# Kernel tuning notes

Hardware: AMD Instinct MI355X
Metric: run time of the kernel (lower is better)

The kernel has to match this reference:

```python
import jax, jax.numpy as jnp
import numpy as np

N = 100000   # num_entities
R = 474      # num_relations (already doubled for inverses)
D = 256      # in_dim == out_dim
E = 1000000  # num edges (first half 'in' mode, second half 'out' mode)
BN_EPS = 1e-5


def setup_inputs() -> dict:
    key = jax.random.key(0)
    ks = jax.random.split(key, 12)
    s = 1.0 / np.sqrt(D)
    return {
        "x": jax.random.normal(ks[0], (N, D), jnp.float32),
        "r": jax.random.normal(ks[1], (R, D), jnp.float32),
        "w_in": jax.random.normal(ks[2], (D, D), jnp.float32) * s,
        "w_out": jax.random.normal(ks[3], (D, D), jnp.float32) * s,
        "w_loop": jax.random.normal(ks[4], (D, D), jnp.float32) * s,
        "w_rel": jax.random.normal(ks[5], (D, D), jnp.float32) * s,
        "loop_rel": jax.random.normal(ks[6], (1, D), jnp.float32),
        "bias": jnp.zeros((D,), jnp.float32),
        "bn_gamma": jnp.ones((D,), jnp.float32),
        "bn_beta": jnp.zeros((D,), jnp.float32),
        "edge_index": jax.random.randint(ks[7], (2, E), 0, N, jnp.int32),
        "edge_type": jax.random.randint(ks[8], (E,), 0, R, jnp.int32),
    }


def reference(x, r, w_in, w_out, w_loop, w_rel, loop_rel, bias,
              bn_gamma, bn_beta, edge_index, edge_type):
    row, col = edge_index[0], edge_index[1]
    # symmetric edge norm 1/(sqrt(D_i) sqrt(D_j)); degrees over all edges
    deg = jax.ops.segment_sum(jnp.ones((E,), x.dtype), row, num_segments=N)
    deg_inv = jnp.where(deg > 0, deg ** -0.5, 0.0)
    norm = deg_inv[row] * deg_inv[col]  # [E]

    r_full = jnp.concatenate([r, loop_rel], axis=0)  # [R+1, D]

    def mode_agg(rw, cl, et, nrm, W):
        # gather -> composition (sub) -> per-mode matmul -> edge-norm -> scatter-add
        composed = x[cl] - r_full[et]                  # [e, D]
        msg = (composed @ W) * nrm[:, None]            # [e, D]
        return jax.ops.segment_sum(msg, rw, num_segments=N)

    half = edge_type.shape[0] // 2
    agg_in = mode_agg(row[:half], col[:half], edge_type[:half], norm[:half], w_in)
    agg_out = mode_agg(row[half:], col[half:], edge_type[half:], norm[half:], w_out)
    # self-loop: every node, relation = loop_rel (no edge norm)
    agg_loop = (x - loop_rel) @ w_loop                 # [N, D]

    h = agg_in + agg_out + agg_loop + bias
    # BatchNorm1d over node dim (batch statistics)
    mean = jnp.mean(h, axis=0)
    var = jnp.var(h, axis=0)
    h = bn_gamma * (h - mean) * jax.lax.rsqrt(var + BN_EPS) + bn_beta
    h = jnp.tanh(h)

    r_out = r @ w_rel  # rel_transformation == 'linear'
    return h, r_out
```

## Files before the change

kernel.cpp:

```cpp
#include <hip/hip_runtime.h>
#include <hip/hip_bf16.h>
#include <stdint.h>

#define D_DIM 256
#define KBIG 768

typedef __attribute__((ext_vector_type(8))) short bf16x8_t;
typedef __attribute__((ext_vector_type(4))) float f32x4_t;
typedef __attribute__((ext_vector_type(2))) float f32x2_t;

__device__ __forceinline__ float bf2f(uint16_t u) {
    union { uint32_t i; float f; } v; v.i = ((uint32_t)u) << 16; return v.f;
}
__device__ __forceinline__ uint16_t f2bf(float f) {
    union { float f; uint32_t i; } v; v.f = f;
    uint32_t x = v.i;
    uint32_t r = (x + 0x7FFFu + ((x >> 16) & 1u)) >> 16;
    return (uint16_t)r;
}
__device__ __forceinline__ uint32_t pack2(float a, float b) {
    return (uint32_t)f2bf(a) | ((uint32_t)f2bf(b) << 16);
}
__device__ __forceinline__ float loadv(const void* base, int f, size_t idx) {
    return f ? ((const float*)base)[idx] : bf2f(((const uint16_t*)base)[idx]);
}
__device__ __forceinline__ float fast_tanh(float x) {
    float t = __builtin_amdgcn_exp2f(x * 2.8853900817779268f);
    return 1.f - 2.f * __builtin_amdgcn_rcpf(t + 1.f);
}
__device__ __forceinline__ f32x2_t up2(uint32_t w) {
    union { uint32_t u[2]; f32x2_t f; } c;
    c.u[0] = w << 16;
    c.u[1] = w & 0xFFFF0000u;
    return c.f;
}
__device__ __forceinline__ void pkfma(f32x2_t& acc, f32x2_t a, f32x2_t b) {
    asm("v_pk_fma_f32 %0, %1, %2, %0" : "+v"(acc) : "v"(a), "v"(b));
}

__device__ __forceinline__ void gll16(const uint16_t* g, uint16_t* l) {
    __builtin_amdgcn_global_load_lds(
        (const __attribute__((address_space(1))) uint32_t*)(const void*)g,
        (__attribute__((address_space(3))) uint32_t*)(void*)l, 16, 0, 0);
}

__global__ void k_detect(const uint32_t* __restrict__ xw, int* __restrict__ flag) {
    int lane = threadIdx.x;
    int c = 0;
#pragma unroll
    for (int j = 0; j < 8; j++) {
        uint32_t w = xw[(size_t)(lane * 8 + j) * 6151];
        uint32_t e = (w >> 7) & 0xFF;
        c += (e >= 100 && e <= 140) ? 1 : 0;
    }
#pragma unroll
    for (int off = 32; off; off >>= 1) c += __shfl_down(c, off);
    if (lane == 0) flag[0] = (c < 128) ? 1 : 0;
}

__global__ __launch_bounds__(256) void k_cast(const void* __restrict__ src,
                                              uint16_t* __restrict__ dst,
                                              int nvec, const int* __restrict__ flagp,
                                              int skip_bf) {
    int f = *flagp;
    int i = blockIdx.x * 256 + threadIdx.x;
    if (i >= nvec) return;
    size_t base = (size_t)i * 8;
    if (f) {
        const float* s = (const float*)src + base;
        float4 a = *(const float4*)s;
        float4 b = *(const float4*)(s + 4);
        uint4 o;
        o.x = (uint32_t)f2bf(a.x) | ((uint32_t)f2bf(a.y) << 16);
        o.y = (uint32_t)f2bf(a.z) | ((uint32_t)f2bf(a.w) << 16);
        o.z = (uint32_t)f2bf(b.x) | ((uint32_t)f2bf(b.y) << 16);
        o.w = (uint32_t)f2bf(b.z) | ((uint32_t)f2bf(b.w) << 16);
        *(uint4*)(dst + base) = o;
    } else {
        if (skip_bf) return;
        *(uint4*)(dst + base) = *(const uint4*)((const uint16_t*)src + base);
    }
}

__global__ void k_transpose(const void* __restrict__ w0, const void* __restrict__ w1,
                            const void* __restrict__ w2, const void* __restrict__ w3,
                            const int* __restrict__ flagp,
                            uint16_t* __restrict__ bt_big, uint16_t* __restrict__ bt_rel) {
    __shared__ uint16_t tile[32][33];
    int f = *flagp;
    int mat = blockIdx.z;
    const void* src = mat == 0 ? w0 : mat == 1 ? w1 : mat == 2 ? w2 : w3;
    int k0 = blockIdx.y * 32, n0 = blockIdx.x * 32;
    int tx = threadIdx.x, ty = threadIdx.y;
    tile[ty][tx] = f2bf(loadv(src, f, (size_t)(k0 + ty) * D_DIM + n0 + tx));
    __syncthreads();
    int n = n0 + ty, k = k0 + tx;
    if (mat < 3) bt_big[(size_t)n * KBIG + mat * D_DIM + k] = tile[tx][ty];
    else         bt_rel[(size_t)n * D_DIM + k] = tile[tx][ty];
}

__global__ void k_cvec(const void* __restrict__ loop_rel, const void* __restrict__ w_loop,
                       const void* __restrict__ bias, const int* __restrict__ flagp,
                       float* __restrict__ cvec) {
    int f = *flagp;
    int c = blockIdx.x;
    int lane = threadIdx.x;
    float s = 0.f;
#pragma unroll
    for (int kk = 0; kk < 4; kk++) {
        int k = kk * 64 + lane;
        s += loadv(loop_rel, f, k) * loadv(w_loop, f, (size_t)k * D_DIM + c);
    }
#pragma unroll
    for (int off = 32; off; off >>= 1) s += __shfl_down(s, off);
    if (lane == 0) cvec[c] = loadv(bias, f, c) - s;
}

__global__ void k_hist(const int* __restrict__ rows, int E, int half,
                       int* __restrict__ deg) {
    int i = blockIdx.x * blockDim.x + threadIdx.x;
    if (i < E) atomicAdd(&deg[rows[i]], (i < half) ? 0x10001 : 1);
}

__global__ void k_scan_a(const int* __restrict__ deg, int N, int* __restrict__ row_start,
                         int* __restrict__ blk_sum, float* __restrict__ dinv) {
    __shared__ int s[1024];
    int t = threadIdx.x;
    int i = blockIdx.x * 1024 + t;
    int v = (i < N) ? (deg[i] & 0xFFFF) : 0;
    if (i < N) dinv[i] = v > 0 ? rsqrtf((float)v) : 0.f;
    s[t] = v;
    __syncthreads();
    for (int off = 1; off < 1024; off <<= 1) {
        int add = (t >= off) ? s[t - off] : 0;
        __syncthreads();
        s[t] += add;
        __syncthreads();
    }
    if (i < N) row_start[i] = s[t] - v;
    if (t == 1023) blk_sum[blockIdx.x] = s[1023];
}

__global__ void k_scan_b(int* __restrict__ blk_sum, int nb) {
    __shared__ int s[128];
    int t = threadIdx.x;
    int v = (t < nb) ? blk_sum[t] : 0;
    s[t] = v;
    __syncthreads();
    for (int off = 1; off < 128; off <<= 1) {
        int add = (t >= off) ? s[t - off] : 0;
        __syncthreads();
        s[t] += add;
        __syncthreads();
    }
    if (t < nb) blk_sum[t] = s[t] - v;
}

__global__ void k_scan_c(int* __restrict__ row_start, const int* __restrict__ blk_sum,
                         const int* __restrict__ degp,
                         int N, int E, int* __restrict__ cur_in, int* __restrict__ cur_out) {
    int i = blockIdx.x * 1024 + threadIdx.x;
    if (i < N) {
        int v = row_start[i] + blk_sum[blockIdx.x];
        row_start[i] = v;
        cur_in[i] = v;
        cur_out[i] = v + (int)(((unsigned)degp[i]) >> 16);
    }
    if (i == 0) row_start[N] = E;
}

__global__ void k_fill(const int* __restrict__ ei, const int* __restrict__ et, int E, int half,
                       int* __restrict__ cur_in, int* __restrict__ cur_out,
                       const float* __restrict__ dinv, uint2* __restrict__ csr) {
    int e = blockIdx.x * blockDim.x + threadIdx.x;
    if (e >= E) return;
    int r_ = ei[e];
    int c_ = ei[E + e];
    int t_ = et[e];
    float w = dinv[r_] * dinv[c_];
    uint32_t m = ((uint32_t)c_ << 9) | (uint32_t)t_;
    int pos = (e < half) ? atomicAdd(&cur_in[r_], 1) : atomicAdd(&cur_out[r_], 1);
    csr[pos] = make_uint2(m, __float_as_uint(w));
}

__global__ __launch_bounds__(256) void k_agg(
    const uint2* __restrict__ csr, const int* __restrict__ row_start,
    const int* __restrict__ degp,
    const void* __restrict__ x_raw, const uint16_t* __restrict__ x_bf,
    const uint16_t* __restrict__ r_bf, const int* __restrict__ flagp,
    uint16_t* __restrict__ s_in, uint16_t* __restrict__ s_out, int N) {
    const char* xb = (const char*)((*flagp) ? x_bf : (const uint16_t*)x_raw);
    const char* rb = (const char*)r_bf;
    int node = blockIdx.x * 4 + (threadIdx.x >> 6);
    int lane = threadIdx.x & 63;
    if (node >= N) return;
    int half = lane >> 5;
    int cob = (lane & 31) * 16;
    int s = row_start[node], e = row_start[node + 1];
    int mid = s + (int)(((unsigned)degp[node]) >> 16);

    f32x2_t ax[4], ar[4];
    float a[8];

#pragma unroll
    for (int k = 0; k < 4; k++) { ax[k] = (f32x2_t){0.f, 0.f}; ar[k] = (f32x2_t){0.f, 0.f}; }
    for (int j = s + half; j < mid; j += 2) {
        uint2 rec = csr[j];
        uint32_t m = rec.x;
        float w = __uint_as_float(rec.y);
        uint4 xv = *(const uint4*)(xb + (m & 0xFFFFFE00u) + cob);
        uint4 rv = *(const uint4*)(rb + ((m & 511u) << 9) + cob);
        f32x2_t w2 = {w, w};
        pkfma(ax[0], up2(xv.x), w2); pkfma(ar[0], up2(rv.x), w2);
        pkfma(ax[1], up2(xv.y), w2); pkfma(ar[1], up2(rv.y), w2);
        pkfma(ax[2], up2(xv.z), w2); pkfma(ar[2], up2(rv.z), w2);
        pkfma(ax[3], up2(xv.w), w2); pkfma(ar[3], up2(rv.w), w2);
    }
#pragma unroll
    for (int k = 0; k < 4; k++) { a[2 * k] = ax[k][0] - ar[k][0]; a[2 * k + 1] = ax[k][1] - ar[k][1]; }
#pragma unroll
    for (int k = 0; k < 8; k++) a[k] += __shfl_xor(a[k], 32);
    if (half == 0) {
        uint4 o;
        o.x = pack2(a[0], a[1]); o.y = pack2(a[2], a[3]);
        o.z = pack2(a[4], a[5]); o.w = pack2(a[6], a[7]);
        *(uint4*)(s_in + (size_t)node * D_DIM + (cob >> 1)) = o;
    }

#pragma unroll
    for (int k = 0; k < 4; k++) { ax[k] = (f32x2_t){0.f, 0.f}; ar[k] = (f32x2_t){0.f, 0.f}; }
    for (int j = mid + half; j < e; j += 2) {
        uint2 rec = csr[j];
        uint32_t m = rec.x;
        float w = __uint_as_float(rec.y);
        uint4 xv = *(const uint4*)(xb + (m & 0xFFFFFE00u) + cob);
        uint4 rv = *(const uint4*)(rb + ((m & 511u) << 9) + cob);
        f32x2_t w2 = {w, w};
        pkfma(ax[0], up2(xv.x), w2); pkfma(ar[0], up2(rv.x), w2);
        pkfma(ax[1], up2(xv.y), w2); pkfma(ar[1], up2(rv.y), w2);
        pkfma(ax[2], up2(xv.z), w2); pkfma(ar[2], up2(rv.z), w2);
        pkfma(ax[3], up2(xv.w), w2); pkfma(ar[3], up2(rv.w), w2);
    }
#pragma unroll
    for (int k = 0; k < 4; k++) { a[2 * k] = ax[k][0] - ar[k][0]; a[2 * k + 1] = ax[k][1] - ar[k][1]; }
#pragma unroll
    for (int k = 0; k < 8; k++) a[k] += __shfl_xor(a[k], 32);
    if (half == 1) {
        uint4 o;
        o.x = pack2(a[0], a[1]); o.y = pack2(a[2], a[3]);
        o.z = pack2(a[4], a[5]); o.w = pack2(a[6], a[7]);
        *(uint4*)(s_out + (size_t)node * D_DIM + (cob >> 1)) = o;
    }
}

__global__ __launch_bounds__(512) void k_gemm(
    const uint16_t* a0, const uint16_t* a1,
    const uint16_t* a2, const uint16_t* a2alt, const int* __restrict__ flagp,
    int M, const uint16_t* __restrict__ bt, int bstride, int ktot,
    const float* __restrict__ addvec, uint16_t* out,
    float* __restrict__ bn_sum, float* __restrict__ bn_sq,
    void* __restrict__ dout2, long long d_off) {
    __shared__ uint16_t As[2][128 * 32];
    __shared__ uint16_t Bs[2][256 * 32];
    int fl = *flagp;
    const uint16_t* a2s = fl ? a2 : a2alt;
    int t = threadIdx.x;
    int mbase = blockIdx.x * 128;
    int wave = t >> 6, lane = t & 63;
    int wm = (wave >> 2) * 64, wn = (wave & 3) * 64;
    int quad = lane >> 4, l15 = lane & 15;

    int roff = lane >> 2, cidx = lane & 3;
    int arowL = wave * 16 + roff;
    int achk = cidx ^ ((arowL >> 1) & 3);
    int agrow = mbase + arowL; if (agrow > M - 1) agrow = M - 1;
    size_t aoff = (size_t)agrow * D_DIM + achk * 8;
    int awoff = (wave * 16) * 32;

    int browL0 = wave * 32 + roff;
    int browL1 = browL0 + 16;
    int bchk0 = cidx ^ ((browL0 >> 1) & 3);
    int bchk1 = cidx ^ ((browL1 >> 1) & 3);
    size_t boff0 = (size_t)browL0 * bstride + bchk0 * 8;
    size_t boff1 = (size_t)browL1 * bstride + bchk1 * 8;
    int bwoff0 = (wave * 32) * 32;
    int bwoff1 = (wave * 32 + 16) * 32;

    int afo[4], bfo[4];
#pragma unroll
    for (int im = 0; im < 4; im++) {
        int row = wm + im * 16 + l15;
        afo[im] = row * 32 + (quad ^ ((row >> 1) & 3)) * 8;
    }
#pragma unroll
    for (int in = 0; in < 4; in++) {
        int row = wn + in * 16 + l15;
        bfo[in] = row * 32 + (quad ^ ((row >> 1) & 3)) * 8;
    }

    f32x4_t acc[4][4];
#pragma unroll
    for (int i = 0; i < 4; i++)
#pragma unroll
        for (int j = 0; j < 4; j++) acc[i][j] = (f32x4_t){0.f, 0.f, 0.f, 0.f};

    auto stage = [&](int buf, int kt) {
        const uint16_t* asec = (kt < 256) ? a0 : (kt < 512 ? a1 : a2s);
        gll16(asec + aoff + (kt & 255), &As[buf][awoff]);
        gll16(bt + boff0 + kt, &Bs[buf][bwoff0]);
        gll16(bt + boff1 + kt, &Bs[buf][bwoff1]);
    };

    stage(0, 0);
    int cur = 0;
    for (int kt = 0; kt < ktot; kt += 32) {
        if (kt + 32 < ktot) {
            stage(cur ^ 1, kt + 32);
            asm volatile("s_waitcnt vmcnt(3)" ::: "memory");
        } else {
            asm volatile("s_waitcnt vmcnt(0)" ::: "memory");
        }
        __builtin_amdgcn_sched_barrier(0);
        __builtin_amdgcn_s_barrier();
        bf16x8_t af[4], bfr[4];
#pragma unroll
        for (int im = 0; im < 4; im++) af[im] = *(const bf16x8_t*)(&As[cur][afo[im]]);
#pragma unroll
        for (int in = 0; in < 4; in++) bfr[in] = *(const bf16x8_t*)(&Bs[cur][bfo[in]]);
#pragma unroll
        for (int im = 0; im < 4; im++)
#pragma unroll
            for (int in = 0; in < 4; in++)
                acc[im][in] = __builtin_amdgcn_mfma_f32_16x16x32_bf16(af[im], bfr[in], acc[im][in], 0, 0, 0);
        asm volatile("s_waitcnt lgkmcnt(0)" ::: "memory");
        __builtin_amdgcn_sched_barrier(0);
        __builtin_amdgcn_s_barrier();
        cur ^= 1;
    }

    float s4[4] = {0.f, 0.f, 0.f, 0.f};
    float q4[4] = {0.f, 0.f, 0.f, 0.f};
#pragma unroll
    for (int im = 0; im < 4; im++) {
#pragma unroll
        for (int in = 0; in < 4; in++) {
            int gn = wn + in * 16 + l15;
            float av_ = addvec ? addvec[gn] : 0.f;
#pragma unroll
            for (int i2 = 0; i2 < 4; i2++) {
                int gm = mbase + wm + im * 16 + quad * 4 + i2;
                if (gm < M) {
                    float val = acc[im][in][i2] + av_;
                    if (dout2) {
                        size_t idx = (size_t)d_off + (size_t)gm * D_DIM + gn;
                        if (fl) ((float*)dout2)[idx] = val;
                        else    ((uint16_t*)dout2)[idx] = f2bf(val);
                    } else {
                        out[(size_t)gm * D_DIM + gn] = f2bf(val);
                    }
                    if (bn_sum) { s4[in] += val; q4[in] += val * val; }
                }
            }
        }
    }
    if (bn_sum) {
        float* sred = (float*)&As[0][0];
        __syncthreads();
        if (t < 256) { sred[t] = 0.f; sred[t + 256] = 0.f; }
        __syncthreads();
#pragma unroll
        for (int in = 0; in < 4; in++) {
            float sv = s4[in], qv = q4[in];
            sv += __shfl_xor(sv, 16); sv += __shfl_xor(sv, 32);
            qv += __shfl_xor(qv, 16); qv += __shfl_xor(qv, 32);
            if (quad == 0) {
                int gn = wn + in * 16 + l15;
                atomicAdd(&sred[gn], sv);
                atomicAdd(&sred[gn + 256], qv);
            }
        }
        __syncthreads();
        if (t < 256) {
            atomicAdd(&bn_sum[t], sred[t]);
            atomicAdd(&bn_sq[t], sred[t + 256]);
        }
    }
}

__global__ __launch_bounds__(256) void k_final(const uint16_t* __restrict__ h_pre,
                                               const float* __restrict__ bn_sum,
                                               const float* __restrict__ bn_sq,
                                               const void* __restrict__ gamma,
                                               const void* __restrict__ beta,
                                               const int* __restrict__ flagp,
                                               int N, void* __restrict__ dout, int total) {
    __shared__ float ssc[256], ssh[256];
    int f = *flagp;
    {
        int c = threadIdx.x;
        float inv_n = 1.f / (float)N;
        float mean = bn_sum[c] * inv_n;
        float var = bn_sq[c] * inv_n - mean * mean;
        float sc = loadv(gamma, f, c) * rsqrtf(var + 1e-5f);
        ssc[c] = sc;
        ssh[c] = loadv(beta, f, c) - mean * sc;
    }
    __syncthreads();
    int t = blockIdx.x * 256 + threadIdx.x;
    int base = t * 8;
    if (base >= total) return;
    int c0 = base & (D_DIM - 1);
    uint4 v = *(const uint4*)(h_pre + base);
    uint16_t e[8];
    e[0] = (uint16_t)(v.x & 0xFFFF); e[1] = (uint16_t)(v.x >> 16);
    e[2] = (uint16_t)(v.y & 0xFFFF); e[3] = (uint16_t)(v.y >> 16);
    e[4] = (uint16_t)(v.z & 0xFFFF); e[5] = (uint16_t)(v.z >> 16);
    e[6] = (uint16_t)(v.w & 0xFFFF); e[7] = (uint16_t)(v.w >> 16);
    float r[8];
#pragma unroll
    for (int i = 0; i < 8; i++)
        r[i] = fast_tanh(bf2f(e[i]) * ssc[c0 + i] + ssh[c0 + i]);
    if (f) {
        float* fo = (float*)dout + base;
        float4 o0 = {r[0], r[1], r[2], r[3]};
        float4 o1 = {r[4], r[5], r[6], r[7]};
        *(float4*)fo = o0;
        *(float4*)(fo + 4) = o1;
    } else {
        uint4 o;
        o.x = (uint32_t)f2bf(r[0]) | ((uint32_t)f2bf(r[1]) << 16);
        o.y = (uint32_t)f2bf(r[2]) | ((uint32_t)f2bf(r[3]) << 16);
        o.z = (uint32_t)f2bf(r[4]) | ((uint32_t)f2bf(r[5]) << 16);
        o.w = (uint32_t)f2bf(r[6]) | ((uint32_t)f2bf(r[7]) << 16);
        *(uint4*)((uint16_t*)dout + base) = o;
    }
}

extern "C" void kernel_launch(void* const* d_in, const int* in_sizes, int n_in,
                              void* d_out, int out_size, void* d_ws, size_t ws_size,
                              hipStream_t stream) {
    const void* x        = d_in[0];
    const void* r        = d_in[1];
    const void* w_in     = d_in[2];
    const void* w_out    = d_in[3];
    const void* w_loop   = d_in[4];
    const void* w_rel    = d_in[5];
    const void* loop_rel = d_in[6];
    const void* bias     = d_in[7];
    const void* bn_gamma = d_in[8];
    const void* bn_beta  = d_in[9];
    const int* edge_index = (const int*)d_in[10];
    const int* edge_type  = (const int*)d_in[11];

    const int N = in_sizes[0] / D_DIM;
    const int R = in_sizes[1] / D_DIM;
    const int E = in_sizes[11];
    const int half = E / 2;

    char* p = (char*)d_ws;
    auto alloc = [&](size_t bytes) -> void* {
        void* q = (void*)p;
        p += (bytes + 255) & ~(size_t)255;
        return q;
    };
    uint16_t* s_out   = (uint16_t*)alloc((size_t)N * D_DIM * 2);
    uint2*    csr     = (uint2*)alloc((size_t)E * 8);
    uint16_t* bt_big  = (uint16_t*)alloc((size_t)D_DIM * KBIG * 2);
    uint16_t* bt_rel  = (uint16_t*)alloc((size_t)D_DIM * D_DIM * 2);
    uint16_t* r_bf    = (uint16_t*)alloc((size_t)R * D_DIM * 2 + 65536);
    int*      deg     = (int*)alloc((size_t)N * 4);
    int*      rstart  = (int*)alloc((size_t)(N + 1) * 4);
    int*      cursor  = (int*)alloc((size_t)N * 4);
    int*      cursor_out = (int*)alloc((size_t)N * 4);
    float*    dinv    = (float*)alloc((size_t)N * 4);
    int*      blksum  = (int*)alloc(128 * 4);
    float*    cvec    = (float*)alloc(D_DIM * 4);
    float*    bn_sum  = (float*)alloc(D_DIM * 4);
    float*    bn_sq   = (float*)alloc(D_DIM * 4);
    int*      dflag   = (int*)alloc(256);
    (void)bn_sq;

    uint16_t* s_in = (uint16_t*)d_out;
    uint16_t* x_bf = (uint16_t*)d_out + (size_t)N * D_DIM;
    uint16_t* h_pre = s_out;

    hipMemsetAsync(deg, 0, (size_t)N * 4, stream);
    hipMemsetAsync(bn_sum, 0, 2 * D_DIM * 4, stream);

    k_detect<<<1, 64, 0, stream>>>((const uint32_t*)x, dflag);
    int xvec = N * D_DIM / 8;
    k_cast<<<(xvec + 255) / 256, 256, 0, stream>>>(x, x_bf, xvec, dflag, 1);
    int rvec = R * D_DIM / 8;
    k_cast<<<(rvec + 255) / 256, 256, 0, stream>>>(r, r_bf, rvec, dflag, 0);
    k_transpose<<<dim3(8, 8, 4), dim3(32, 32), 0, stream>>>(w_in, w_out, w_loop, w_rel,
                                                            dflag, bt_big, bt_rel);
    k_cvec<<<D_DIM, 64, 0, stream>>>(loop_rel, w_loop, bias, dflag, cvec);

    int eb = (E + 255) / 256;
    k_hist<<<eb, 256, 0, stream>>>(edge_index, E, half, deg);
    int nb = (N + 1023) / 1024;
    k_scan_a<<<nb, 1024, 0, stream>>>(deg, N, rstart, blksum, dinv);
    k_scan_b<<<1, 128, 0, stream>>>(blksum, nb);
    k_scan_c<<<nb, 1024, 0, stream>>>(rstart, blksum, deg, N, E, cursor, cursor_out);
    k_fill<<<eb, 256, 0, stream>>>(edge_index, edge_type, E, half, cursor, cursor_out,
                                   dinv, csr);

    k_agg<<<(N + 3) / 4, 256, 0, stream>>>(csr, rstart, deg, x, x_bf, r_bf, dflag,
                                           s_in, s_out, N);

    int gx = (N + 127) / 128;
    k_gemm<<<gx, 512, 0, stream>>>(s_in, s_out, x_bf, (const uint16_t*)x, dflag,
                                   N, bt_big, KBIG, KBIG, cvec, h_pre, bn_sum, bn_sq,
                                   nullptr, 0);
    int gr_ = (R + 127) / 128;
    k_gemm<<<gr_, 512, 0, stream>>>(r_bf, r_bf, r_bf, r_bf, dflag,
                                    R, bt_rel, D_DIM, D_DIM, nullptr, nullptr,
                                    nullptr, nullptr,
                                    d_out, (long long)N * D_DIM);

    int total = N * D_DIM;
    k_final<<<(total / 8 + 255) / 256, 256, 0, stream>>>(h_pre, bn_sum, bn_sq,
                                                         bn_gamma, bn_beta, dflag,
                                                         N, d_out, total);
}
```

Before: 529.4 us.

## Replace LDS-staged GEMM with direct global-to-register double-buffered MFMA loads

The GEMM kernel stops staging A and B tiles in shared memory with global_load_lds and barriers. Each wave now loads its MFMA fragments straight from global memory into registers, double-buffered across k-steps. The block tile shrinks from 128x256 to 64x256 with 256 threads, and launch bounds now request 3 blocks per CU. This removes LDS traffic and per-step barriers, but each wave re-reads the shared A rows from global or L2 with less coalesced 16-byte accesses, and register pressure rises.

```diff
diff --git a/kernel.cpp b/kernel.cpp
--- a/kernel.cpp
+++ b/kernel.cpp
@@ -36,12 +36,6 @@
 }
 __device__ __forceinline__ void pkfma(f32x2_t& acc, f32x2_t a, f32x2_t b) {
     asm("v_pk_fma_f32 %0, %1, %2, %0" : "+v"(acc) : "v"(a), "v"(b));
-}
-
-__device__ __forceinline__ void gll16(const uint16_t* g, uint16_t* l) {
-    __builtin_amdgcn_global_load_lds(
-        (const __attribute__((address_space(1))) uint32_t*)(const void*)g,
-        (__attribute__((address_space(3))) uint32_t*)(void*)l, 16, 0, 0);
 }
 
 __global__ void k_detect(const uint32_t* __restrict__ xw, int* __restrict__ flag) {
@@ -253,49 +247,32 @@
     }
 }
 
-__global__ __launch_bounds__(512) void k_gemm(
+__global__ __launch_bounds__(256, 3) void k_gemm(
     const uint16_t* a0, const uint16_t* a1,
     const uint16_t* a2, const uint16_t* a2alt, const int* __restrict__ flagp,
     int M, const uint16_t* __restrict__ bt, int bstride, int ktot,
     const float* __restrict__ addvec, uint16_t* out,
     float* __restrict__ bn_sum, float* __restrict__ bn_sq,
     void* __restrict__ dout2, long long d_off) {
-    __shared__ uint16_t As[2][128 * 32];
-    __shared__ uint16_t Bs[2][256 * 32];
+    __shared__ float sred[512];
     int fl = *flagp;
     const uint16_t* a2s = fl ? a2 : a2alt;
     int t = threadIdx.x;
-    int mbase = blockIdx.x * 128;
+    int mbase = blockIdx.x * 64;
     int wave = t >> 6, lane = t & 63;
-    int wm = (wave >> 2) * 64, wn = (wave & 3) * 64;
+    int wn = wave * 64;
     int quad = lane >> 4, l15 = lane & 15;
 
-    int roff = lane >> 2, cidx = lane & 3;
-    int arowL = wave * 16 + roff;
-    int achk = cidx ^ ((arowL >> 1) & 3);
-    int agrow = mbase + arowL; if (agrow > M - 1) agrow = M - 1;
-    size_t aoff = (size_t)agrow * D_DIM + achk * 8;
-    int awoff = (wave * 16) * 32;
-
-    int browL0 = wave * 32 + roff;
-    int browL1 = browL0 + 16;
-    int bchk0 = cidx ^ ((browL0 >> 1) & 3);
-    int bchk1 = cidx ^ ((browL1 >> 1) & 3);
-    size_t boff0 = (size_t)browL0 * bstride + bchk0 * 8;
-    size_t boff1 = (size_t)browL1 * bstride + bchk1 * 8;
-    int bwoff0 = (wave * 32) * 32;
-    int bwoff1 = (wave * 32 + 16) * 32;
-
-    int afo[4], bfo[4];
+    size_t aoff[4], boff[4];
 #pragma unroll
     for (int im = 0; im < 4; im++) {
-        int row = wm + im * 16 + l15;
-        afo[im] = row * 32 + (quad ^ ((row >> 1) & 3)) * 8;
+        int grow = mbase + im * 16 + l15;
+        if (grow > M - 1) grow = M - 1;
+        aoff[im] = (size_t)grow * D_DIM + quad * 8;
     }
 #pragma unroll
     for (int in = 0; in < 4; in++) {
-        int row = wn + in * 16 + l15;
-        bfo[in] = row * 32 + (quad ^ ((row >> 1) & 3)) * 8;
+        boff[in] = (size_t)(wn + in * 16 + l15) * bstride + quad * 8;
     }
 
     f32x4_t acc[4][4];
@@ -304,38 +281,38 @@
 #pragma unroll
         for (int j = 0; j < 4; j++) acc[i][j] = (f32x4_t){0.f, 0.f, 0.f, 0.f};
 
-    auto stage = [&](int buf, int kt) {
-        const uint16_t* asec = (kt < 256) ? a0 : (kt < 512 ? a1 : a2s);
-        gll16(asec + aoff + (kt & 255), &As[buf][awoff]);
-        gll16(bt + boff0 + kt, &Bs[buf][bwoff0]);
-        gll16(bt + boff1 + kt, &Bs[buf][bwoff1]);
+    auto loadA = [&](bf16x8_t* a, int kt) {
+        const uint16_t* base = (kt < 256) ? a0 : (kt < 512 ? a1 : a2s);
+        int ko = kt & 255;
+#pragma unroll
+        for (int im = 0; im < 4; im++)
+            a[im] = *(const bf16x8_t*)(base + aoff[im] + ko);
     };
-
-    stage(0, 0);
-    int cur = 0;
-    for (int kt = 0; kt < ktot; kt += 32) {
-        if (kt + 32 < ktot) {
-            stage(cur ^ 1, kt + 32);
-            asm volatile("s_waitcnt vmcnt(3)" ::: "memory");
-        } else {
-            asm volatile("s_waitcnt vmcnt(0)" ::: "memory");
-        }
-        __builtin_amdgcn_sched_barrier(0);
-        __builtin_amdgcn_s_barrier();
-        bf16x8_t af[4], bfr[4];
-#pragma unroll
-        for (int im = 0; im < 4; im++) af[im] = *(const bf16x8_t*)(&As[cur][afo[im]]);
-#pragma unroll
-        for (int in = 0; in < 4; in++) bfr[in] = *(const bf16x8_t*)(&Bs[cur][bfo[in]]);
+    auto loadB = [&](bf16x8_t* b, int kt) {
+#pragma unroll
+        for (int in = 0; in < 4; in++)
+            b[in] = *(const bf16x8_t*)(bt + boff[in] + kt);
+    };
+    auto compute = [&](bf16x8_t* a, bf16x8_t* b) {
 #pragma unroll
         for (int im = 0; im < 4; im++)
 #pragma unroll
             for (int in = 0; in < 4; in++)
-                acc[im][in] = __builtin_amdgcn_mfma_f32_16x16x32_bf16(af[im], bfr[in], acc[im][in], 0, 0, 0);
-        asm volatile("s_waitcnt lgkmcnt(0)" ::: "memory");
-        __builtin_amdgcn_sched_barrier(0);
-        __builtin_amdgcn_s_barrier();
-        cur ^= 1;
+                acc[im][in] = __builtin_amdgcn_mfma_f32_16x16x32_bf16(a[im], b[in], acc[im][in], 0, 0, 0);
+    };
+
+    bf16x8_t ca[4], cb[4], na[4], nb[4];
+    loadA(ca, 0); loadB(cb, 0);
+    int kt = 0;
+    for (;;) {
+        if (kt + 32 < ktot) { loadA(na, kt + 32); loadB(nb, kt + 32); }
+        compute(ca, cb);
+        kt += 32;
+        if (kt >= ktot) break;
+        if (kt + 32 < ktot) { loadA(ca, kt + 32); loadB(cb, kt + 32); }
+        compute(na, nb);
+        kt += 32;
+        if (kt >= ktot) break;
     }
 
     float s4[4] = {0.f, 0.f, 0.f, 0.f};
@@ -348,7 +325,7 @@
             float av_ = addvec ? addvec[gn] : 0.f;
 #pragma unroll
             for (int i2 = 0; i2 < 4; i2++) {
-                int gm = mbase + wm + im * 16 + quad * 4 + i2;
+                int gm = mbase + im * 16 + quad * 4 + i2;
                 if (gm < M) {
                     float val = acc[im][in][i2] + av_;
                     if (dout2) {
@@ -364,8 +341,6 @@
         }
     }
     if (bn_sum) {
-        float* sred = (float*)&As[0][0];
-        __syncthreads();
         if (t < 256) { sred[t] = 0.f; sred[t + 256] = 0.f; }
         __syncthreads();
 #pragma unroll
@@ -508,12 +483,12 @@
     k_agg<<<(N + 3) / 4, 256, 0, stream>>>(csr, rstart, deg, x, x_bf, r_bf, dflag,
                                            s_in, s_out, N);
 
-    int gx = (N + 127) / 128;
-    k_gemm<<<gx, 512, 0, stream>>>(s_in, s_out, x_bf, (const uint16_t*)x, dflag,
+    int gx = (N + 63) / 64;
+    k_gemm<<<gx, 256, 0, stream>>>(s_in, s_out, x_bf, (const uint16_t*)x, dflag,
                                    N, bt_big, KBIG, KBIG, cvec, h_pre, bn_sum, bn_sq,
                                    nullptr, 0);
-    int gr_ = (R + 127) / 128;
-    k_gemm<<<gr_, 512, 0, stream>>>(r_bf, r_bf, r_bf, r_bf, dflag,
+    int gr_ = (R + 63) / 64;
+    k_gemm<<<gr_, 256, 0, stream>>>(r_bf, r_bf, r_bf, r_bf, dflag,
                                     R, bt_rel, D_DIM, D_DIM, nullptr, nullptr,
                                     nullptr, nullptr,
                                     d_out, (long long)N * D_DIM);
```

Measured after the change: 627.7 us. 1.19x slower.

## Shrink GEMM tile to 64 rows single-buffered and fold block-sum scan into scan_c

Applied to the files above, without the earlier changes.

The GEMM kernel moves from 128-row tiles with 512 threads and double-buffered LDS to 64-row tiles with 256 threads and a single LDS buffer. Each wave now covers all 64 rows and its own 64-column slice, and launch bounds ask for 6 blocks per CU. This trades the explicit prefetch/compute overlap for lower LDS use and more resident blocks, aiming to hide latency through occupancy, while the B operand is reloaded twice as often per output row. Separately, the single-block scan of block sums is folded into scan_c: each block redundantly scans the 128 sums, which removes one kernel launch.

```diff
diff --git a/kernel.cpp b/kernel.cpp
--- a/kernel.cpp
+++ b/kernel.cpp
@@ -141,27 +141,30 @@
     if (t == 1023) blk_sum[blockIdx.x] = s[1023];
 }
 
-__global__ void k_scan_b(int* __restrict__ blk_sum, int nb) {
+__global__ void k_scan_c(int* __restrict__ row_start, const int* __restrict__ blk_sum,
+                         const int* __restrict__ degp,
+                         int N, int E, int nb,
+                         int* __restrict__ cur_in, int* __restrict__ cur_out) {
     __shared__ int s[128];
+    __shared__ int myoff;
     int t = threadIdx.x;
-    int v = (t < nb) ? blk_sum[t] : 0;
-    s[t] = v;
+    int v0 = 0;
+    if (t < 128) {
+        v0 = (t < nb) ? blk_sum[t] : 0;
+        s[t] = v0;
+    }
     __syncthreads();
     for (int off = 1; off < 128; off <<= 1) {
-        int add = (t >= off) ? s[t - off] : 0;
-        __syncthreads();
-        s[t] += add;
-        __syncthreads();
-    }
-    if (t < nb) blk_sum[t] = s[t] - v;
-}
-
-__global__ void k_scan_c(int* __restrict__ row_start, const int* __restrict__ blk_sum,
-                         const int* __restrict__ degp,
-                         int N, int E, int* __restrict__ cur_in, int* __restrict__ cur_out) {
-    int i = blockIdx.x * 1024 + threadIdx.x;
+        int add = (t < 128 && t >= off) ? s[t - off] : 0;
+        __syncthreads();
+        if (t < 128) s[t] += add;
+        __syncthreads();
+    }
+    if (t == blockIdx.x) myoff = s[t] - v0;
+    __syncthreads();
+    int i = blockIdx.x * 1024 + t;
     if (i < N) {
-        int v = row_start[i] + blk_sum[blockIdx.x];
+        int v = row_start[i] + myoff;
         row_start[i] = v;
         cur_in[i] = v;
         cur_out[i] = v + (int)(((unsigned)degp[i]) >> 16);
@@ -253,21 +256,21 @@
     }
 }
 
-__global__ __launch_bounds__(512) void k_gemm(
+__global__ __launch_bounds__(256, 6) void k_gemm(
     const uint16_t* a0, const uint16_t* a1,
     const uint16_t* a2, const uint16_t* a2alt, const int* __restrict__ flagp,
     int M, const uint16_t* __restrict__ bt, int bstride, int ktot,
     const float* __restrict__ addvec, uint16_t* out,
     float* __restrict__ bn_sum, float* __restrict__ bn_sq,
     void* __restrict__ dout2, long long d_off) {
-    __shared__ uint16_t As[2][128 * 32];
-    __shared__ uint16_t Bs[2][256 * 32];
+    __shared__ uint16_t As[64 * 32];
+    __shared__ uint16_t Bs[256 * 32];
     int fl = *flagp;
     const uint16_t* a2s = fl ? a2 : a2alt;
     int t = threadIdx.x;
-    int mbase = blockIdx.x * 128;
+    int mbase = blockIdx.x * 64;
     int wave = t >> 6, lane = t & 63;
-    int wm = (wave >> 2) * 64, wn = (wave & 3) * 64;
+    int wn = wave * 64;
     int quad = lane >> 4, l15 = lane & 15;
 
     int roff = lane >> 2, cidx = lane & 3;
@@ -275,21 +278,22 @@
     int achk = cidx ^ ((arowL >> 1) & 3);
     int agrow = mbase + arowL; if (agrow > M - 1) agrow = M - 1;
     size_t aoff = (size_t)agrow * D_DIM + achk * 8;
-    int awoff = (wave * 16) * 32;
-
-    int browL0 = wave * 32 + roff;
-    int browL1 = browL0 + 16;
-    int bchk0 = cidx ^ ((browL0 >> 1) & 3);
-    int bchk1 = cidx ^ ((browL1 >> 1) & 3);
-    size_t boff0 = (size_t)browL0 * bstride + bchk0 * 8;
-    size_t boff1 = (size_t)browL1 * bstride + bchk1 * 8;
-    int bwoff0 = (wave * 32) * 32;
-    int bwoff1 = (wave * 32 + 16) * 32;
+    uint16_t* aldsb = &As[(wave * 16) * 32];
+
+    size_t boff[4];
+    uint16_t* bldsb[4];
+#pragma unroll
+    for (int c = 0; c < 4; c++) {
+        int row = wave * 64 + c * 16 + roff;
+        int chk = cidx ^ ((row >> 1) & 3);
+        boff[c] = (size_t)row * bstride + chk * 8;
+        bldsb[c] = &Bs[(wave * 64 + c * 16) * 32];
+    }
 
     int afo[4], bfo[4];
 #pragma unroll
     for (int im = 0; im < 4; im++) {
-        int row = wm + im * 16 + l15;
+        int row = im * 16 + l15;
         afo[im] = row * 32 + (quad ^ ((row >> 1) & 3)) * 8;
     }
 #pragma unroll
@@ -304,38 +308,24 @@
 #pragma unroll
         for (int j = 0; j < 4; j++) acc[i][j] = (f32x4_t){0.f, 0.f, 0.f, 0.f};
 
-    auto stage = [&](int buf, int kt) {
+    for (int kt = 0; kt < ktot; kt += 32) {
         const uint16_t* asec = (kt < 256) ? a0 : (kt < 512 ? a1 : a2s);
-        gll16(asec + aoff + (kt & 255), &As[buf][awoff]);
-        gll16(bt + boff0 + kt, &Bs[buf][bwoff0]);
-        gll16(bt + boff1 + kt, &Bs[buf][bwoff1]);
-    };
-
-    stage(0, 0);
-    int cur = 0;
-    for (int kt = 0; kt < ktot; kt += 32) {
-        if (kt + 32 < ktot) {
-            stage(cur ^ 1, kt + 32);
-            asm volatile("s_waitcnt vmcnt(3)" ::: "memory");
-        } else {
-            asm volatile("s_waitcnt vmcnt(0)" ::: "memory");
-        }
-        __builtin_amdgcn_sched_barrier(0);
-        __builtin_amdgcn_s_barrier();
+        int klocal = kt & 255;
+        gll16(asec + aoff + klocal, aldsb);
+#pragma unroll
+        for (int c = 0; c < 4; c++) gll16(bt + boff[c] + kt, bldsb[c]);
+        __syncthreads();
         bf16x8_t af[4], bfr[4];
 #pragma unroll
-        for (int im = 0; im < 4; im++) af[im] = *(const bf16x8_t*)(&As[cur][afo[im]]);
-#pragma unroll
-        for (int in = 0; in < 4; in++) bfr[in] = *(const bf16x8_t*)(&Bs[cur][bfo[in]]);
+        for (int im = 0; im < 4; im++) af[im] = *(const bf16x8_t*)(&As[afo[im]]);
+#pragma unroll
+        for (int in = 0; in < 4; in++) bfr[in] = *(const bf16x8_t*)(&Bs[bfo[in]]);
 #pragma unroll
         for (int im = 0; im < 4; im++)
 #pragma unroll
             for (int in = 0; in < 4; in++)
                 acc[im][in] = __builtin_amdgcn_mfma_f32_16x16x32_bf16(af[im], bfr[in], acc[im][in], 0, 0, 0);
-        asm volatile("s_waitcnt lgkmcnt(0)" ::: "memory");
-        __builtin_amdgcn_sched_barrier(0);
-        __builtin_amdgcn_s_barrier();
-        cur ^= 1;
+        __syncthreads();
     }
 
     float s4[4] = {0.f, 0.f, 0.f, 0.f};
@@ -348,7 +338,7 @@
             float av_ = addvec ? addvec[gn] : 0.f;
 #pragma unroll
             for (int i2 = 0; i2 < 4; i2++) {
-                int gm = mbase + wm + im * 16 + quad * 4 + i2;
+                int gm = mbase + im * 16 + quad * 4 + i2;
                 if (gm < M) {
                     float val = acc[im][in][i2] + av_;
                     if (dout2) {
@@ -364,9 +354,8 @@
         }
     }
     if (bn_sum) {
-        float* sred = (float*)&As[0][0];
-        __syncthreads();
-        if (t < 256) { sred[t] = 0.f; sred[t + 256] = 0.f; }
+        float* sred = (float*)As;
+        sred[t] = 0.f; sred[t + 256] = 0.f;
         __syncthreads();
 #pragma unroll
         for (int in = 0; in < 4; in++) {
@@ -380,10 +369,8 @@
             }
         }
         __syncthreads();
-        if (t < 256) {
-            atomicAdd(&bn_sum[t], sred[t]);
-            atomicAdd(&bn_sq[t], sred[t + 256]);
-        }
+        atomicAdd(&bn_sum[t], sred[t]);
+        atomicAdd(&bn_sq[t], sred[t + 256]);
     }
 }
 
@@ -500,20 +487,19 @@
     k_hist<<<eb, 256, 0, stream>>>(edge_index, E, half, deg);
     int nb = (N + 1023) / 1024;
     k_scan_a<<<nb, 1024, 0, stream>>>(deg, N, rstart, blksum, dinv);
-    k_scan_b<<<1, 128, 0, stream>>>(blksum, nb);
-    k_scan_c<<<nb, 1024, 0, stream>>>(rstart, blksum, deg, N, E, cursor, cursor_out);
+    k_scan_c<<<nb, 1024, 0, stream>>>(rstart, blksum, deg, N, E, nb, cursor, cursor_out);
     k_fill<<<eb, 256, 0, stream>>>(edge_index, edge_type, E, half, cursor, cursor_out,
                                    dinv, csr);
 
     k_agg<<<(N + 3) / 4, 256, 0, stream>>>(csr, rstart, deg, x, x_bf, r_bf, dflag,
                                            s_in, s_out, N);
 
-    int gx = (N + 127) / 128;
-    k_gemm<<<gx, 512, 0, stream>>>(s_in, s_out, x_bf, (const uint16_t*)x, dflag,
+    int gx = (N + 63) / 64;
+    k_gemm<<<gx, 256, 0, stream>>>(s_in, s_out, x_bf, (const uint16_t*)x, dflag,
                                    N, bt_big, KBIG, KBIG, cvec, h_pre, bn_sum, bn_sq,
                                    nullptr, 0);
-    int gr_ = (R + 127) / 128;
-    k_gemm<<<gr_, 512, 0, stream>>>(r_bf, r_bf, r_bf, r_bf, dflag,
+    int gr_ = (R + 63) / 64;
+    k_gemm<<<gr_, 256, 0, stream>>>(r_bf, r_bf, r_bf, r_bf, dflag,
                                     R, bt_rel, D_DIM, D_DIM, nullptr, nullptr,
                                     nullptr, nullptr,
                                     d_out, (long long)N * D_DIM);
```

Measured after the change: 788.7 us. +49.0%, slower.
